# Kernel optimization log

Hardware: AMD Instinct MI355X
Metric: run time of the kernel (lower is better)

The kernel has to match this reference:

```python
import jax, jax.numpy as jnp
import numpy as np

H_OUT = 16   # RoIRotate(height=16)
MAX_W = 192  # static pad width; setup bounds aspect so int(aspect*H_OUT) <= 184 < MAX_W


def setup_inputs() -> dict:
    key = jax.random.key(0)
    k1, k2, k3, k4, k5 = jax.random.split(key, 5)
    B, C, H, W, N = 4, 32, 512, 512, 64
    image = jax.random.normal(k1, (B, C, H, W), dtype=jnp.float32)
    left = jax.random.uniform(k2, (B, N), minval=0.0, maxval=W - 80.0)
    top = jax.random.uniform(k3, (B, N), minval=0.0, maxval=H - 80.0)
    bh = jax.random.uniform(k4, (B, N), minval=12.0, maxval=64.0)
    aspect = jax.random.uniform(k5, (B, N), minval=1.0, maxval=11.5)
    bw = aspect * bh
    theta = jnp.zeros((B, N), dtype=jnp.float32)  # present in box format, unused by forward
    boxes = jnp.stack([left, top, left + bw, top + bh, theta], axis=-1)
    return {"image": image, "boxes": boxes}


def _bilinear(img, x, y):
    # img: [C,H,W]; x,y: [N,Ho,Wo] sample coordinates (pixel units)
    C, H, W = img.shape
    x0 = jnp.clip(jnp.floor(x).astype(jnp.int32), 0, W - 1)
    x1 = jnp.clip(jnp.floor(x).astype(jnp.int32) + 1, 0, W - 1)
    y0 = jnp.clip(jnp.floor(y).astype(jnp.int32), 0, H - 1)
    y1 = jnp.clip(jnp.floor(y).astype(jnp.int32) + 1, 0, H - 1)
    ia = img[:, y0, x0]  # [C,N,Ho,Wo]
    ib = img[:, y1, x0]
    ic = img[:, y0, x1]
    idd = img[:, y1, x1]
    x0f, x1f = x0.astype(x.dtype), x1.astype(x.dtype)
    y0f, y1f = y0.astype(y.dtype), y1.astype(y.dtype)
    wa = (x1f - x) * (y1f - y)
    wb = (x1f - x) * (y - y0f)
    wc = (x - x0f) * (y1f - y)
    wd = (x - x0f) * (y - y0f)
    return ia * wa + ib * wb + ic * wc + idd * wd  # [C,N,Ho,Wo]


def reference(image, boxes):
    # image: [B,C,H,W]; boxes: [B,N,5] = (left, top, right, bottom, theta)
    B, C, H, W = image.shape
    N = boxes.shape[1]
    left, top = boxes[..., 0], boxes[..., 1]
    bw = boxes[..., 2] - boxes[..., 0]
    bh = boxes[..., 3] - boxes[..., 1]
    # per-box output width = int(aspect * height) (positive -> trunc == floor)
    width = (bw / bh * H_OUT).astype(jnp.int32)            # [B,N]
    each_w = bw / (width - 1).astype(jnp.float32)          # [B,N]
    each_h = bh / jnp.float32(H_OUT - 1)                   # [B,N]
    xx = jnp.arange(MAX_W, dtype=jnp.float32)[None, None, :] * each_w[..., None] + left[..., None]  # [B,N,MAX_W]
    yy = jnp.arange(H_OUT, dtype=jnp.float32)[None, None, :] * each_h[..., None] + top[..., None]   # [B,N,H_OUT]
    X = jnp.broadcast_to(xx[:, :, None, :], (B, N, H_OUT, MAX_W))
    Y = jnp.broadcast_to(yy[:, :, :, None], (B, N, H_OUT, MAX_W))
    samp = jax.vmap(_bilinear)(image, X, Y)                # [B,C,N,H_OUT,MAX_W]
    result = jnp.transpose(samp, (0, 2, 1, 3, 4))          # [B,N,C,H_OUT,MAX_W]
    colmask = jnp.arange(MAX_W)[None, None, :] < width[..., None]  # [B,N,MAX_W]
    result = result * colmask[:, :, None, None, :].astype(result.dtype)
    mask = colmask.astype(jnp.uint8)                       # [B,N,MAX_W]
    return result, mask
```

## Files before the change

### kernel.cpp

```cpp
#include <hip/hip_runtime.h>

namespace {
constexpr int kB = 4, kC = 32, kH = 512, kW = 512, kN = 64;
constexpr int kHout = 16, kMaxW = 192;
constexpr long long kResultElems = (long long)kB * kN * kC * kHout * kMaxW;
}

extern "C" __global__ __launch_bounds__(kMaxW) void roi_rotate(
    const float* __restrict__ image,
    const float* __restrict__ boxes,
    float* __restrict__ result,
    float* __restrict__ mask)
{
    __shared__ float ls[2][2][kW];

    const int blk = blockIdx.x;
    const int i  = blk & (kHout - 1);
    const int bn = blk >> 4;
    const int b  = bn >> 6;

    const float* bx = boxes + bn * 5;
    const float left = bx[0];
    const float top  = bx[1];
    const float bw   = __fsub_rn(bx[2], bx[0]);
    const float bh   = __fsub_rn(bx[3], bx[1]);
    const int width  = (int)(__fmul_rn(__fdiv_rn(bw, bh), (float)kHout));
    const float each_w = __fdiv_rn(bw, (float)(width - 1));
    const float each_h = __fdiv_rn(bh, (float)(kHout - 1));

    const int j = threadIdx.x;
    const float x = __fadd_rn(__fmul_rn((float)j, each_w), left);
    const float y = __fadd_rn(__fmul_rn((float)i, each_h), top);

    const int xf = (int)floorf(x);
    const int yf = (int)floorf(y);
    const int x0 = min(max(xf,     0), kW - 1);
    const int x1 = min(max(xf + 1, 0), kW - 1);
    const int y0 = min(max(yf,     0), kH - 1);
    const int y1 = min(max(yf + 1, 0), kH - 1);

    const float wx1 = (float)x1 - x;
    const float wx0 = x - (float)x0;
    const float wy1 = (float)y1 - y;
    const float wy0 = y - (float)y0;
    const float wa = wx1 * wy1;
    const float wb = wx1 * wy0;
    const float wc = wx0 * wy1;
    const float wd = wx0 * wy0;

    const bool valid = (j < width);

    const int xlo = (min(max((int)floorf(left), 0), kW - 1)) & ~3;
    const int xhi = min((int)floorf(__fadd_rn(left, bw)) + 1, kW - 1);
    const int S    = xhi - xlo + 1;
    const int nvec = (S + 3) >> 2;

    const bool do_stage = (j < nvec);
    const size_t row_off0 = (size_t)y0 * kW + xlo;
    const size_t row_off1 = (size_t)y1 * kW + xlo;
    const int lx0 = x0 - xlo;
    const int lx1 = x1 - xlo;

    float* op = result + (size_t)bn * (kC * kHout * kMaxW) + (size_t)i * kMaxW + j;
    const float* chbase = image + (size_t)b * ((size_t)kC * kH * kW);
    constexpr size_t kChStride = (size_t)kH * kW;
    constexpr int kOpStride = kHout * kMaxW;

    for (int c = 0; c < kC; c += 2) {
        const float* p0 = chbase + (size_t)c * kChStride;
        const float* p1 = p0 + kChStride;
        if (do_stage) {
            const int o = 4 * j;
            const float4 v00 = *(const float4*)(p0 + row_off0 + o);
            const float4 v01 = *(const float4*)(p0 + row_off1 + o);
            const float4 v10 = *(const float4*)(p1 + row_off0 + o);
            const float4 v11 = *(const float4*)(p1 + row_off1 + o);
            *(float4*)&ls[0][0][o] = v00;
            *(float4*)&ls[0][1][o] = v01;
            *(float4*)&ls[1][0][o] = v10;
            *(float4*)&ls[1][1][o] = v11;
        }
        __syncthreads();
        float out0 = 0.0f, out1 = 0.0f;
        if (valid) {
            out0 = ls[0][0][lx0] * wa + ls[0][1][lx0] * wb
                 + ls[0][0][lx1] * wc + ls[0][1][lx1] * wd;
            out1 = ls[1][0][lx0] * wa + ls[1][1][lx0] * wb
                 + ls[1][0][lx1] * wc + ls[1][1][lx1] * wd;
        }
        op[0]         = out0;
        op[kOpStride] = out1;
        op += 2 * kOpStride;
        __syncthreads();
    }

    if (i == 0) {
        mask[bn * kMaxW + j] = valid ? 1.0f : 0.0f;
    }
}

extern "C" void kernel_launch(void* const* d_in, const int* in_sizes, int n_in,
                              void* d_out, int out_size, void* d_ws, size_t ws_size,
                              hipStream_t stream) {
    const float* image = (const float*)d_in[0];
    const float* boxes = (const float*)d_in[1];
    float* result = (float*)d_out;
    float* mask   = result + kResultElems;

    dim3 grid(kB * kN * kHout);
    dim3 block(kMaxW);
    hipLaunchKernelGGL(roi_rotate, grid, block, 0, stream,
                       image, boxes, result, mask);
}
```

Baseline: 224.4 us.

## Prefetch next channel group into registers and process four channels per barrier

```diff
diff --git a/kernel.cpp b/kernel.cpp
--- a/kernel.cpp
+++ b/kernel.cpp
@@ -4,6 +4,7 @@
 constexpr int kB = 4, kC = 32, kH = 512, kW = 512, kN = 64;
 constexpr int kHout = 16, kMaxW = 192;
 constexpr long long kResultElems = (long long)kB * kN * kC * kHout * kMaxW;
+constexpr int kCP = 4;
 }
 
 extern "C" __global__ __launch_bounds__(kMaxW) void roi_rotate(
@@ -12,7 +13,7 @@
     float* __restrict__ result,
     float* __restrict__ mask)
 {
-    __shared__ float ls[2][2][kW];
+    __shared__ float ls[kCP][2][kW];
 
     const int blk = blockIdx.x;
     const int i  = blk & (kHout - 1);
@@ -56,8 +57,9 @@
     const int nvec = (S + 3) >> 2;
 
     const bool do_stage = (j < nvec);
-    const size_t row_off0 = (size_t)y0 * kW + xlo;
-    const size_t row_off1 = (size_t)y1 * kW + xlo;
+    const int o = 4 * j;
+    const size_t row_off0 = (size_t)y0 * kW + xlo + o;
+    const size_t row_off1 = (size_t)y1 * kW + xlo + o;
     const int lx0 = x0 - xlo;
     const int lx1 = x1 - xlo;
 
@@ -66,31 +68,42 @@
     constexpr size_t kChStride = (size_t)kH * kW;
     constexpr int kOpStride = kHout * kMaxW;
 
-    for (int c = 0; c < kC; c += 2) {
-        const float* p0 = chbase + (size_t)c * kChStride;
-        const float* p1 = p0 + kChStride;
+    float4 r[kCP][2];
+    if (do_stage) {
+        #pragma unroll
+        for (int cc = 0; cc < kCP; ++cc) {
+            const float* p = chbase + (size_t)cc * kChStride;
+            r[cc][0] = *(const float4*)(p + row_off0);
+            r[cc][1] = *(const float4*)(p + row_off1);
+        }
+    }
+
+    for (int c = 0; c < kC; c += kCP) {
         if (do_stage) {
-            const int o = 4 * j;
-            const float4 v00 = *(const float4*)(p0 + row_off0 + o);
-            const float4 v01 = *(const float4*)(p0 + row_off1 + o);
-            const float4 v10 = *(const float4*)(p1 + row_off0 + o);
-            const float4 v11 = *(const float4*)(p1 + row_off1 + o);
-            *(float4*)&ls[0][0][o] = v00;
-            *(float4*)&ls[0][1][o] = v01;
-            *(float4*)&ls[1][0][o] = v10;
-            *(float4*)&ls[1][1][o] = v11;
+            #pragma unroll
+            for (int cc = 0; cc < kCP; ++cc) {
+                *(float4*)&ls[cc][0][o] = r[cc][0];
+                *(float4*)&ls[cc][1][o] = r[cc][1];
+            }
+            if (c + kCP < kC) {
+                #pragma unroll
+                for (int cc = 0; cc < kCP; ++cc) {
+                    const float* p = chbase + (size_t)(c + kCP + cc) * kChStride;
+                    r[cc][0] = *(const float4*)(p + row_off0);
+                    r[cc][1] = *(const float4*)(p + row_off1);
+                }
+            }
         }
         __syncthreads();
-        float out0 = 0.0f, out1 = 0.0f;
-        if (valid) {
-            out0 = ls[0][0][lx0] * wa + ls[0][1][lx0] * wb
-                 + ls[0][0][lx1] * wc + ls[0][1][lx1] * wd;
-            out1 = ls[1][0][lx0] * wa + ls[1][1][lx0] * wb
-                 + ls[1][0][lx1] * wc + ls[1][1][lx1] * wd;
+        #pragma unroll
+        for (int cc = 0; cc < kCP; ++cc) {
+            float out = 0.0f;
+            if (valid) {
+                out = ls[cc][0][lx0] * wa + ls[cc][1][lx0] * wb
+                    + ls[cc][0][lx1] * wc + ls[cc][1][lx1] * wd;
+            }
+            op[(c + cc) * kOpStride] = out;
         }
-        op[0]         = out0;
-        op[kOpStride] = out1;
-        op += 2 * kOpStride;
         __syncthreads();
     }
 
```

New measurement: 291.1 us. 29.8% more time.
